# Performance work log

Hardware: AMD Instinct MI355X
Metric: run time of the kernel (lower is better)

## Reference

```python
import jax, jax.numpy as jnp
import numpy as np

HEADS = 16
ROT_DIM = 32  # RotaryEmbedding(dim=32), interleaved (GPT-J style) as in rotary_embedding_torch
THETA = 10000.0


def _rope(x):
    # x: (B, H, S, hd); rotate first ROT_DIM dims, pass through the rest
    S = x.shape[-2]
    inv_freq = 1.0 / (THETA ** (jnp.arange(0, ROT_DIM, 2, dtype=jnp.float32) / ROT_DIM))  # (ROT_DIM/2,)
    ang = jnp.arange(S, dtype=jnp.float32)[:, None] * inv_freq[None, :]                   # (S, ROT_DIM/2)
    ang = jnp.repeat(ang, 2, axis=-1)                                                     # (S, ROT_DIM) interleaved
    cos, sin = jnp.cos(ang), jnp.sin(ang)
    xr, xp = x[..., :ROT_DIM], x[..., ROT_DIM:]
    # rotate_half, interleaved pairs: (x1, x2) -> (-x2, x1)
    x2 = xr.reshape(*xr.shape[:-1], ROT_DIM // 2, 2)
    xr_half = jnp.stack([-x2[..., 1], x2[..., 0]], axis=-1).reshape(xr.shape)
    xr = xr * cos + xr_half * sin
    return jnp.concatenate([xr, xp], axis=-1)


def _split_heads(x, H):
    # (S, B, D) -> (B, H, S, hd)
    S, B, D = x.shape
    return x.transpose(1, 0, 2).reshape(B, S, H, D // H).transpose(0, 2, 1, 3)


def setup_inputs() -> dict:
    key = jax.random.key(0)
    ks = jax.random.split(key, 11)
    S, B, D = 2048, 2, 1024
    f = lambda k, shp, s=1.0: jax.random.normal(k, shp, dtype=jnp.float32) * s
    return {
        "Q": f(ks[0], (S, B, D)),
        "K": f(ks[1], (S, B, D)),
        "V": f(ks[2], (S, B, D)),
        "Wq": f(ks[3], (D, D), 0.02), "bq": f(ks[4], (D,), 0.02),
        "Wk": f(ks[5], (D, D), 0.02), "bk": f(ks[6], (D,), 0.02),
        "Wv": f(ks[7], (D, D), 0.02), "bv": f(ks[8], (D,), 0.02),
        "Wo": f(ks[9], (D, D), 0.02), "bo": f(ks[10], (D,), 0.02),
    }


def reference(Q, K, V, Wq, bq, Wk, bk, Wv, bv, Wo, bo):
    S, B, D = Q.shape
    H = HEADS
    hd = D // H
    q = _rope(_split_heads(Q @ Wq.T + bq, H))   # (B, H, S, hd)
    k = _rope(_split_heads(K @ Wk.T + bk, H))
    v = _split_heads(V @ Wv.T + bv, H)
    scores = jnp.einsum("bhqd,bhkd->bhqk", q, k) / jnp.sqrt(jnp.float32(hd))
    probs = jax.nn.softmax(scores, axis=-1)
    out = jnp.einsum("bhqk,bhkd->bhqd", probs, v)  # (B, H, S, hd)
    out = out.transpose(0, 2, 1, 3).reshape(B, S, D).transpose(1, 0, 2)  # (S, B, D)
    return out @ Wo.T + bo
```

## Files before the change

kernel.cpp:

```cpp
#include <hip/hip_runtime.h>
#include <hip/hip_bf16.h>
#include <hip/hip_fp16.h>

#define S_LEN  2048
#define BATCH  2
#define DMODEL 1024
#define NHEADS 16
#define HD     64
#define MROWS  4096
#define LD     72

using f16 = _Float16;
typedef __attribute__((ext_vector_type(8))) _Float16 f16x8;
typedef __attribute__((ext_vector_type(4))) _Float16 f16x4;
typedef __attribute__((ext_vector_type(4))) float    f32x4;

__global__ __launch_bounds__(256) void rope_table(float* __restrict__ rc, float* __restrict__ rs)
{
    int idx = blockIdx.x * 256 + threadIdx.x;
    int s = idx >> 4, i = idx & 15;
    float inv = powf(10000.0f, -(float)(2 * i) / 32.0f);
    float ang = (float)s * inv;
    rc[idx] = cosf(ang);
    rs[idx] = sinf(ang);
}

__global__ __launch_bounds__(256) void proj_gemm(
    const float* __restrict__ Xq, const float* __restrict__ Xk, const float* __restrict__ Xv,
    const float* __restrict__ Wq, const float* __restrict__ Wk, const float* __restrict__ Wv,
    const float* __restrict__ bq, const float* __restrict__ bk, const float* __restrict__ bv,
    f16* __restrict__ qo, f16* __restrict__ ko, f16* __restrict__ vo,
    const float* __restrict__ rc, const float* __restrict__ rs)
{
    const int mode = blockIdx.z;
    const float* X    = (mode == 0) ? Xq : (mode == 1) ? Xk : Xv;
    const float* W    = (mode == 0) ? Wq : (mode == 1) ? Wk : Wv;
    const float* bias = (mode == 0) ? bq : (mode == 1) ? bk : bv;

    __shared__ f16 Al[128 * 40];
    __shared__ f16 Bl[128 * 40];

    const int t = threadIdx.x;
    const int lane = t & 63, wid = t >> 6;
    const int wr = wid >> 1, wc = wid & 1;
    const int m0 = blockIdx.x * 128, n0 = blockIdx.y * 128;

    f32x4 acc[4][4];
    #pragma unroll
    for (int m = 0; m < 4; m++)
        #pragma unroll
        for (int n = 0; n < 4; n++)
            acc[m][n] = f32x4{0.f, 0.f, 0.f, 0.f};

    for (int k0 = 0; k0 < DMODEL; k0 += 32) {
        __syncthreads();
        #pragma unroll
        for (int i = 0; i < 2; i++) {
            int e = (i * 256 + t) * 8;
            int r = e >> 5, c = e & 31;
            {
                const float* src = &X[(size_t)(m0 + r) * DMODEL + k0 + c];
                float4 v0 = *reinterpret_cast<const float4*>(src);
                float4 v1 = *reinterpret_cast<const float4*>(src + 4);
                f16x8 h = { (f16)v0.x, (f16)v0.y, (f16)v0.z, (f16)v0.w,
                            (f16)v1.x, (f16)v1.y, (f16)v1.z, (f16)v1.w };
                *reinterpret_cast<f16x8*>(&Al[r * 40 + c]) = h;
            }
            {
                const float* src = &W[(size_t)(n0 + r) * DMODEL + k0 + c];
                float4 v0 = *reinterpret_cast<const float4*>(src);
                float4 v1 = *reinterpret_cast<const float4*>(src + 4);
                f16x8 h = { (f16)v0.x, (f16)v0.y, (f16)v0.z, (f16)v0.w,
                            (f16)v1.x, (f16)v1.y, (f16)v1.z, (f16)v1.w };
                *reinterpret_cast<f16x8*>(&Bl[r * 40 + c]) = h;
            }
        }
        __syncthreads();
        f16x8 a[4], b[4];
        #pragma unroll
        for (int m = 0; m < 4; m++)
            a[m] = *reinterpret_cast<const f16x8*>(&Al[(wr * 64 + m * 16 + (lane & 15)) * 40 + (lane >> 4) * 8]);
        #pragma unroll
        for (int n = 0; n < 4; n++)
            b[n] = *reinterpret_cast<const f16x8*>(&Bl[(wc * 64 + n * 16 + (lane & 15)) * 40 + (lane >> 4) * 8]);
        #pragma unroll
        for (int m = 0; m < 4; m++)
            #pragma unroll
            for (int n = 0; n < 4; n++)
                acc[m][n] = __builtin_amdgcn_mfma_f32_16x16x32_f16(a[m], b[n], acc[m][n], 0, 0, 0);
    }

    const int rowb = m0 + wr * 64, colb = n0 + wc * 64;
    #pragma unroll
    for (int n = 0; n < 4; n++) {
        int cN = colb + n * 16 + (lane & 15);
        float bvv = bias[cN];
        int h = cN >> 6, d = cN & 63;
        #pragma unroll
        for (int m = 0; m < 4; m++) {
            #pragma unroll
            for (int rg = 0; rg < 4; rg++) {
                int r = rowb + m * 16 + (lane >> 4) * 4 + rg;
                int s = r >> 1, bi = r & 1;
                float val = acc[m][n][rg] + bvv;
                if (mode < 2) {
                    float pv = __shfl_xor(val, 1);
                    if (d < 32) {
                        int fi = d >> 1;
                        float cc = rc[s * 16 + fi], ss = rs[s * 16 + fi];
                        val = ((d & 1) == 0) ? val * cc - pv * ss : val * cc + pv * ss;
                    }
                    if (mode == 0) val *= 0.18033688f;
                    ((mode == 0) ? qo : ko)[(((size_t)bi * NHEADS + h) * S_LEN + s) * HD + d] = (f16)val;
                } else {
                    vo[(((size_t)bi * NHEADS + h) * HD + d) * S_LEN + s] = (f16)val;
                }
            }
        }
    }
}

__global__ __launch_bounds__(512) void attn_fwd(
    const f16* __restrict__ qb, const f16* __restrict__ kb,
    const f16* __restrict__ vt, f16* __restrict__ ctx)
{
    __shared__ f16 Kl[64 * LD];
    __shared__ f16 Vl[64 * LD];
    __shared__ f16 Pl[8 * 16 * LD];

    const int t = threadIdx.x, lane = t & 63, wid = t >> 6;
    const int q15 = lane & 15, g = lane >> 4;
    const int bh = blockIdx.y;
    const int q0 = blockIdx.x * 128 + wid * 16;

    const f16* qptr = qb + ((size_t)bh * S_LEN + q0) * HD;
    f16x8 qf0 = *reinterpret_cast<const f16x8*>(&qptr[q15 * HD + g * 8]);
    f16x8 qf1 = *reinterpret_cast<const f16x8*>(&qptr[q15 * HD + g * 8 + 32]);

    f32x4 ctxa[4];
    #pragma unroll
    for (int i = 0; i < 4; i++) ctxa[i] = f32x4{0.f, 0.f, 0.f, 0.f};
    float mrun = -3.0e38f, lrun = 0.f;

    const int r_st = t >> 3, c_st = (t & 7) * 8;
    const f16* kg = kb + (size_t)bh * S_LEN * HD + (size_t)r_st * HD + c_st;
    const f16* vg = vt + (size_t)bh * HD * S_LEN + (size_t)r_st * S_LEN + c_st;
    f16* kl_st = &Kl[r_st * LD + c_st];
    f16* vl_st = &Vl[r_st * LD + c_st];
    f16* pbase = &Pl[wid * (16 * LD)];

    for (int kt = 0; kt < S_LEN / 64; kt++) {
        __syncthreads();
        *reinterpret_cast<uint4*>(kl_st) = *reinterpret_cast<const uint4*>(kg);
        *reinterpret_cast<uint4*>(vl_st) = *reinterpret_cast<const uint4*>(vg);
        kg += 64 * HD;
        vg += 64;
        __syncthreads();

        f32x4 sc[4];
        __builtin_amdgcn_s_setprio(1);
        #pragma unroll
        for (int f = 0; f < 4; f++) {
            f16x8 kf0 = *reinterpret_cast<const f16x8*>(&Kl[(f * 16 + q15) * LD + g * 8]);
            f16x8 kf1 = *reinterpret_cast<const f16x8*>(&Kl[(f * 16 + q15) * LD + g * 8 + 32]);
            f32x4 z = {0.f, 0.f, 0.f, 0.f};
            z = __builtin_amdgcn_mfma_f32_16x16x32_f16(kf0, qf0, z, 0, 0, 0);
            sc[f] = __builtin_amdgcn_mfma_f32_16x16x32_f16(kf1, qf1, z, 0, 0, 0);
        }
        __builtin_amdgcn_s_setprio(0);

        float pmf[4];
        #pragma unroll
        for (int f = 0; f < 4; f++)
            pmf[f] = fmaxf(fmaxf(sc[f][0], sc[f][1]), fmaxf(sc[f][2], sc[f][3]));
        float pmax = fmaxf(fmaxf(pmf[0], pmf[1]), fmaxf(pmf[2], pmf[3]));
        pmax = fmaxf(pmax, __shfl_xor(pmax, 16));
        pmax = fmaxf(pmax, __shfl_xor(pmax, 32));
        float mnew = fmaxf(mrun, pmax);
        float scale = __builtin_amdgcn_exp2f(mrun - mnew);
        float tsum = 0.f;
        #pragma unroll
        for (int f = 0; f < 4; f++)
            #pragma unroll
            for (int rg = 0; rg < 4; rg++) {
                float p = __builtin_amdgcn_exp2f(sc[f][rg] - mnew);
                sc[f][rg] = p;
                tsum += p;
            }
        tsum += __shfl_xor(tsum, 16);
        tsum += __shfl_xor(tsum, 32);
        lrun = lrun * scale + tsum;
        mrun = mnew;
        #pragma unroll
        for (int n = 0; n < 4; n++) {
            ctxa[n][0] *= scale; ctxa[n][1] *= scale;
            ctxa[n][2] *= scale; ctxa[n][3] *= scale;
        }

        #pragma unroll
        for (int f = 0; f < 4; f++) {
            f16x4 pw = { (f16)sc[f][0], (f16)sc[f][1], (f16)sc[f][2], (f16)sc[f][3] };
            *reinterpret_cast<f16x4*>(&pbase[q15 * LD + f * 16 + g * 4]) = pw;
        }
        asm volatile("s_waitcnt lgkmcnt(0)" ::: "memory");
        __builtin_amdgcn_sched_barrier(0);

        __builtin_amdgcn_s_setprio(1);
        #pragma unroll
        for (int c = 0; c < 2; c++) {
            f16x8 pfr = *reinterpret_cast<const f16x8*>(&pbase[q15 * LD + g * 8 + c * 32]);
            #pragma unroll
            for (int n = 0; n < 4; n++) {
                f16x8 vf = *reinterpret_cast<const f16x8*>(&Vl[(n * 16 + q15) * LD + g * 8 + c * 32]);
                ctxa[n] = __builtin_amdgcn_mfma_f32_16x16x32_f16(vf, pfr, ctxa[n], 0, 0, 0);
            }
        }
        __builtin_amdgcn_s_setprio(0);
    }

    const int bi = bh >> 4, h = bh & 15;
    const int s = q0 + q15;
    float inv = 1.0f / lrun;
    f16* outp = &ctx[((size_t)s * BATCH + bi) * DMODEL + h * HD];
    #pragma unroll
    for (int n = 0; n < 4; n++) {
        f16x4 o = { (f16)(ctxa[n][0] * inv), (f16)(ctxa[n][1] * inv),
                    (f16)(ctxa[n][2] * inv), (f16)(ctxa[n][3] * inv) };
        *reinterpret_cast<f16x4*>(&outp[n * 16 + g * 4]) = o;
    }
}

__global__ __launch_bounds__(256) void out_gemm(
    const f16* __restrict__ X, const float* __restrict__ W,
    const float* __restrict__ bias, float* __restrict__ out)
{
    __shared__ f16 Al[128 * 40];
    __shared__ f16 Bl[128 * 40];

    const int t = threadIdx.x;
    const int lane = t & 63, wid = t >> 6;
    const int wr = wid >> 1, wc = wid & 1;
    const int m0 = blockIdx.x * 128, n0 = blockIdx.y * 128;

    f32x4 acc[4][4];
    #pragma unroll
    for (int m = 0; m < 4; m++)
        #pragma unroll
        for (int n = 0; n < 4; n++)
            acc[m][n] = f32x4{0.f, 0.f, 0.f, 0.f};

    for (int k0 = 0; k0 < DMODEL; k0 += 32) {
        __syncthreads();
        #pragma unroll
        for (int i = 0; i < 2; i++) {
            int e = (i * 256 + t) * 8;
            int r = e >> 5, c = e & 31;
            *reinterpret_cast<uint4*>(&Al[r * 40 + c]) =
                *reinterpret_cast<const uint4*>(&X[(size_t)(m0 + r) * DMODEL + k0 + c]);
            {
                const float* src = &W[(size_t)(n0 + r) * DMODEL + k0 + c];
                float4 v0 = *reinterpret_cast<const float4*>(src);
                float4 v1 = *reinterpret_cast<const float4*>(src + 4);
                f16x8 h = { (f16)v0.x, (f16)v0.y, (f16)v0.z, (f16)v0.w,
                            (f16)v1.x, (f16)v1.y, (f16)v1.z, (f16)v1.w };
                *reinterpret_cast<f16x8*>(&Bl[r * 40 + c]) = h;
            }
        }
        __syncthreads();
        f16x8 a[4], b[4];
        #pragma unroll
        for (int m = 0; m < 4; m++)
            a[m] = *reinterpret_cast<const f16x8*>(&Al[(wr * 64 + m * 16 + (lane & 15)) * 40 + (lane >> 4) * 8]);
        #pragma unroll
        for (int n = 0; n < 4; n++)
            b[n] = *reinterpret_cast<const f16x8*>(&Bl[(wc * 64 + n * 16 + (lane & 15)) * 40 + (lane >> 4) * 8]);
        #pragma unroll
        for (int m = 0; m < 4; m++)
            #pragma unroll
            for (int n = 0; n < 4; n++)
                acc[m][n] = __builtin_amdgcn_mfma_f32_16x16x32_f16(a[m], b[n], acc[m][n], 0, 0, 0);
    }

    const int rowb = m0 + wr * 64, colb = n0 + wc * 64;
    #pragma unroll
    for (int n = 0; n < 4; n++) {
        int cN = colb + n * 16 + (lane & 15);
        float bvv = bias[cN];
        #pragma unroll
        for (int m = 0; m < 4; m++) {
            #pragma unroll
            for (int rg = 0; rg < 4; rg++) {
                int r = rowb + m * 16 + (lane >> 4) * 4 + rg;
                out[(size_t)r * DMODEL + cN] = acc[m][n][rg] + bvv;
            }
        }
    }
}

extern "C" void kernel_launch(void* const* d_in, const int* in_sizes, int n_in,
                              void* d_out, int out_size, void* d_ws, size_t ws_size,
                              hipStream_t stream)
{
    const float* Q  = (const float*)d_in[0];
    const float* K  = (const float*)d_in[1];
    const float* V  = (const float*)d_in[2];
    const float* Wq = (const float*)d_in[3];
    const float* bq = (const float*)d_in[4];
    const float* Wk = (const float*)d_in[5];
    const float* bk = (const float*)d_in[6];
    const float* Wv = (const float*)d_in[7];
    const float* bv = (const float*)d_in[8];
    const float* Wo = (const float*)d_in[9];
    const float* bo = (const float*)d_in[10];
    float* out = (float*)d_out;

    char* w = (char*)d_ws;
    const size_t szT = (size_t)S_LEN * 16 * sizeof(float);
    const size_t szQ = (size_t)MROWS * DMODEL * sizeof(f16);
    float* rc  = (float*)(w);
    float* rs  = (float*)(w + szT);
    f16* qbuf = (f16*)(w + 2 * szT);
    f16* kbuf = (f16*)(w + 2 * szT + szQ);
    f16* vtb  = (f16*)(w + 2 * szT + 2 * szQ);
    f16* ctxb = (f16*)(w + 2 * szT + 3 * szQ);

    rope_table<<<(S_LEN * 16) / 256, 256, 0, stream>>>(rc, rs);

    proj_gemm<<<dim3(MROWS / 128, DMODEL / 128, 3), 256, 0, stream>>>(
        Q, K, V, Wq, Wk, Wv, bq, bk, bv, qbuf, kbuf, vtb, rc, rs);

    attn_fwd<<<dim3(S_LEN / 128, BATCH * NHEADS), 512, 0, stream>>>(qbuf, kbuf, vtb, ctxb);

    out_gemm<<<dim3(MROWS / 128, DMODEL / 128), 256, 0, stream>>>(ctxb, Wo, bo, out);
}
```

Before: 169.0 us.

## Pre-convert inputs and weights to fp16 and use async LDS-load GEMMs

Adds a conversion kernel that casts Q/K/V and all four weight matrices to fp16 in workspace. New projection and output GEMMs then load fp16 tiles directly into LDS with global_load_lds, replacing the fp32 load-and-convert staging. This is meant to halve GEMM input bandwidth and drop per-tile conversion work. The cost is an extra pass over about 64MB of fp32 data plus a workspace-size-dependent code path, with the old path kept as fallback.

```diff
diff --git a/kernel.cpp b/kernel.cpp
--- a/kernel.cpp
+++ b/kernel.cpp
@@ -15,6 +15,12 @@
 typedef __attribute__((ext_vector_type(4))) _Float16 f16x4;
 typedef __attribute__((ext_vector_type(4))) float    f32x4;
 
+__device__ __forceinline__ void gload16(const void* g, void* l)
+{
+    __builtin_amdgcn_global_load_lds((const __attribute__((address_space(1))) void*)g,
+                                     (__attribute__((address_space(3))) void*)l, 16, 0, 0);
+}
+
 __global__ __launch_bounds__(256) void rope_table(float* __restrict__ rc, float* __restrict__ rs)
 {
     int idx = blockIdx.x * 256 + threadIdx.x;
@@ -23,6 +29,185 @@
     float ang = (float)s * inv;
     rc[idx] = cosf(ang);
     rs[idx] = sinf(ang);
+}
+
+__global__ __launch_bounds__(256) void cvt_all(
+    const float* __restrict__ Q, const float* __restrict__ K, const float* __restrict__ V,
+    const float* __restrict__ Wq, const float* __restrict__ Wk, const float* __restrict__ Wv,
+    const float* __restrict__ Wo, f16* __restrict__ dst)
+{
+    const int z = blockIdx.y;
+    const float* src; size_t off; int n8;
+    switch (z) {
+        case 0:  src = Q;  off = 0;        n8 = 524288; break;
+        case 1:  src = K;  off = 4194304;  n8 = 524288; break;
+        case 2:  src = V;  off = 8388608;  n8 = 524288; break;
+        case 3:  src = Wq; off = 12582912; n8 = 131072; break;
+        case 4:  src = Wk; off = 13631488; n8 = 131072; break;
+        case 5:  src = Wv; off = 14680064; n8 = 131072; break;
+        default: src = Wo; off = 15728640; n8 = 131072; break;
+    }
+    int i = blockIdx.x * 256 + threadIdx.x;
+    if (i >= n8) return;
+    const float4* s = reinterpret_cast<const float4*>(src) + (size_t)i * 2;
+    float4 v0 = s[0], v1 = s[1];
+    f16x8 h = { (f16)v0.x, (f16)v0.y, (f16)v0.z, (f16)v0.w,
+                (f16)v1.x, (f16)v1.y, (f16)v1.z, (f16)v1.w };
+    reinterpret_cast<f16x8*>(dst + off)[i] = h;
+}
+
+__global__ __launch_bounds__(256) void proj_gemm_h(
+    const f16* __restrict__ Xq, const f16* __restrict__ Xk, const f16* __restrict__ Xv,
+    const f16* __restrict__ Wq, const f16* __restrict__ Wk, const f16* __restrict__ Wv,
+    const float* __restrict__ bq, const float* __restrict__ bk, const float* __restrict__ bv,
+    f16* __restrict__ qo, f16* __restrict__ ko, f16* __restrict__ vo,
+    const float* __restrict__ rc, const float* __restrict__ rs)
+{
+    const int mode = blockIdx.z;
+    const f16* X     = (mode == 0) ? Xq : (mode == 1) ? Xk : Xv;
+    const f16* W     = (mode == 0) ? Wq : (mode == 1) ? Wk : Wv;
+    const float* bias = (mode == 0) ? bq : (mode == 1) ? bk : bv;
+
+    __shared__ f16 Al[128 * 32];
+    __shared__ f16 Bl[128 * 32];
+
+    const int t = threadIdx.x, lane = t & 63, wid = t >> 6;
+    const int q15 = lane & 15, g = lane >> 4;
+    const int wr = wid >> 1, wc = wid & 1;
+    const int m0 = blockIdx.x * 128, n0 = blockIdx.y * 128;
+
+    const int srow = wid * 16 + (lane >> 2);
+    const int scol = (lane & 3) * 8;
+    const f16* Xg = X + (size_t)(m0 + srow) * DMODEL + scol;
+    const f16* Wg = W + (size_t)(n0 + srow) * DMODEL + scol;
+    f16* al0 = &Al[(wid * 16) * 32];
+    f16* al1 = &Al[(wid * 16 + 64) * 32];
+    f16* bl0 = &Bl[(wid * 16) * 32];
+    f16* bl1 = &Bl[(wid * 16 + 64) * 32];
+
+    f32x4 acc[4][4];
+    #pragma unroll
+    for (int m = 0; m < 4; m++)
+        #pragma unroll
+        for (int n = 0; n < 4; n++)
+            acc[m][n] = f32x4{0.f, 0.f, 0.f, 0.f};
+
+    for (int k0 = 0; k0 < DMODEL; k0 += 32) {
+        __syncthreads();
+        gload16(Xg + k0, al0);
+        gload16(Xg + (size_t)64 * DMODEL + k0, al1);
+        gload16(Wg + k0, bl0);
+        gload16(Wg + (size_t)64 * DMODEL + k0, bl1);
+        __syncthreads();
+
+        f16x8 a[4], b[4];
+        #pragma unroll
+        for (int m = 0; m < 4; m++)
+            a[m] = *reinterpret_cast<const f16x8*>(&Al[(wr * 64 + m * 16 + q15) * 32 + g * 8]);
+        #pragma unroll
+        for (int n = 0; n < 4; n++)
+            b[n] = *reinterpret_cast<const f16x8*>(&Bl[(wc * 64 + n * 16 + q15) * 32 + g * 8]);
+        #pragma unroll
+        for (int m = 0; m < 4; m++)
+            #pragma unroll
+            for (int n = 0; n < 4; n++)
+                acc[m][n] = __builtin_amdgcn_mfma_f32_16x16x32_f16(a[m], b[n], acc[m][n], 0, 0, 0);
+    }
+
+    const int rowb = m0 + wr * 64, colb = n0 + wc * 64;
+    #pragma unroll
+    for (int n = 0; n < 4; n++) {
+        int cN = colb + n * 16 + q15;
+        float bvv = bias[cN];
+        int h = cN >> 6, d = cN & 63;
+        #pragma unroll
+        for (int m = 0; m < 4; m++) {
+            #pragma unroll
+            for (int rg = 0; rg < 4; rg++) {
+                int r = rowb + m * 16 + g * 4 + rg;
+                int s = r >> 1, bi = r & 1;
+                float val = acc[m][n][rg] + bvv;
+                if (mode < 2) {
+                    float pv = __shfl_xor(val, 1);
+                    if (d < 32) {
+                        int fi = d >> 1;
+                        float cc = rc[s * 16 + fi], ss = rs[s * 16 + fi];
+                        val = ((d & 1) == 0) ? val * cc - pv * ss : val * cc + pv * ss;
+                    }
+                    if (mode == 0) val *= 0.18033688f;
+                    ((mode == 0) ? qo : ko)[(((size_t)bi * NHEADS + h) * S_LEN + s) * HD + d] = (f16)val;
+                } else {
+                    vo[(((size_t)bi * NHEADS + h) * HD + d) * S_LEN + s] = (f16)val;
+                }
+            }
+        }
+    }
+}
+
+__global__ __launch_bounds__(256) void out_gemm_h(
+    const f16* __restrict__ X, const f16* __restrict__ W,
+    const float* __restrict__ bias, float* __restrict__ out)
+{
+    __shared__ f16 Al[128 * 32];
+    __shared__ f16 Bl[128 * 32];
+
+    const int t = threadIdx.x, lane = t & 63, wid = t >> 6;
+    const int q15 = lane & 15, g = lane >> 4;
+    const int wr = wid >> 1, wc = wid & 1;
+    const int m0 = blockIdx.x * 128, n0 = blockIdx.y * 128;
+
+    const int srow = wid * 16 + (lane >> 2);
+    const int scol = (lane & 3) * 8;
+    const f16* Xg = X + (size_t)(m0 + srow) * DMODEL + scol;
+    const f16* Wg = W + (size_t)(n0 + srow) * DMODEL + scol;
+    f16* al0 = &Al[(wid * 16) * 32];
+    f16* al1 = &Al[(wid * 16 + 64) * 32];
+    f16* bl0 = &Bl[(wid * 16) * 32];
+    f16* bl1 = &Bl[(wid * 16 + 64) * 32];
+
+    f32x4 acc[4][4];
+    #pragma unroll
+    for (int m = 0; m < 4; m++)
+        #pragma unroll
+        for (int n = 0; n < 4; n++)
+            acc[m][n] = f32x4{0.f, 0.f, 0.f, 0.f};
+
+    for (int k0 = 0; k0 < DMODEL; k0 += 32) {
+        __syncthreads();
+        gload16(Xg + k0, al0);
+        gload16(Xg + (size_t)64 * DMODEL + k0, al1);
+        gload16(Wg + k0, bl0);
+        gload16(Wg + (size_t)64 * DMODEL + k0, bl1);
+        __syncthreads();
+
+        f16x8 a[4], b[4];
+        #pragma unroll
+        for (int m = 0; m < 4; m++)
+            a[m] = *reinterpret_cast<const f16x8*>(&Al[(wr * 64 + m * 16 + q15) * 32 + g * 8]);
+        #pragma unroll
+        for (int n = 0; n < 4; n++)
+            b[n] = *reinterpret_cast<const f16x8*>(&Bl[(wc * 64 + n * 16 + q15) * 32 + g * 8]);
+        #pragma unroll
+        for (int m = 0; m < 4; m++)
+            #pragma unroll
+            for (int n = 0; n < 4; n++)
+                acc[m][n] = __builtin_amdgcn_mfma_f32_16x16x32_f16(a[m], b[n], acc[m][n], 0, 0, 0);
+    }
+
+    const int rowb = m0 + wr * 64, colb = n0 + wc * 64;
+    #pragma unroll
+    for (int n = 0; n < 4; n++) {
+        int cN = colb + n * 16 + q15;
+        float bvv = bias[cN];
+        #pragma unroll
+        for (int m = 0; m < 4; m++) {
+            #pragma unroll
+            for (int rg = 0; rg < 4; rg++) {
+                int r = rowb + m * 16 + g * 4 + rg;
+                out[(size_t)r * DMODEL + cN] = acc[m][n][rg] + bvv;
+            }
+        }
+    }
 }
 
 __global__ __launch_bounds__(256) void proj_gemm(
@@ -120,116 +305,6 @@
     }
 }
 
-__global__ __launch_bounds__(512) void attn_fwd(
-    const f16* __restrict__ qb, const f16* __restrict__ kb,
-    const f16* __restrict__ vt, f16* __restrict__ ctx)
-{
-    __shared__ f16 Kl[64 * LD];
-    __shared__ f16 Vl[64 * LD];
-    __shared__ f16 Pl[8 * 16 * LD];
-
-    const int t = threadIdx.x, lane = t & 63, wid = t >> 6;
-    const int q15 = lane & 15, g = lane >> 4;
-    const int bh = blockIdx.y;
-    const int q0 = blockIdx.x * 128 + wid * 16;
-
-    const f16* qptr = qb + ((size_t)bh * S_LEN + q0) * HD;
-    f16x8 qf0 = *reinterpret_cast<const f16x8*>(&qptr[q15 * HD + g * 8]);
-    f16x8 qf1 = *reinterpret_cast<const f16x8*>(&qptr[q15 * HD + g * 8 + 32]);
-
-    f32x4 ctxa[4];
-    #pragma unroll
-    for (int i = 0; i < 4; i++) ctxa[i] = f32x4{0.f, 0.f, 0.f, 0.f};
-    float mrun = -3.0e38f, lrun = 0.f;
-
-    const int r_st = t >> 3, c_st = (t & 7) * 8;
-    const f16* kg = kb + (size_t)bh * S_LEN * HD + (size_t)r_st * HD + c_st;
-    const f16* vg = vt + (size_t)bh * HD * S_LEN + (size_t)r_st * S_LEN + c_st;
-    f16* kl_st = &Kl[r_st * LD + c_st];
-    f16* vl_st = &Vl[r_st * LD + c_st];
-    f16* pbase = &Pl[wid * (16 * LD)];
-
-    for (int kt = 0; kt < S_LEN / 64; kt++) {
-        __syncthreads();
-        *reinterpret_cast<uint4*>(kl_st) = *reinterpret_cast<const uint4*>(kg);
-        *reinterpret_cast<uint4*>(vl_st) = *reinterpret_cast<const uint4*>(vg);
-        kg += 64 * HD;
-        vg += 64;
-        __syncthreads();
-
-        f32x4 sc[4];
-        __builtin_amdgcn_s_setprio(1);
-        #pragma unroll
-        for (int f = 0; f < 4; f++) {
-            f16x8 kf0 = *reinterpret_cast<const f16x8*>(&Kl[(f * 16 + q15) * LD + g * 8]);
-            f16x8 kf1 = *reinterpret_cast<const f16x8*>(&Kl[(f * 16 + q15) * LD + g * 8 + 32]);
-            f32x4 z = {0.f, 0.f, 0.f, 0.f};
-            z = __builtin_amdgcn_mfma_f32_16x16x32_f16(kf0, qf0, z, 0, 0, 0);
-            sc[f] = __builtin_amdgcn_mfma_f32_16x16x32_f16(kf1, qf1, z, 0, 0, 0);
-        }
-        __builtin_amdgcn_s_setprio(0);
-
-        float pmf[4];
-        #pragma unroll
-        for (int f = 0; f < 4; f++)
-            pmf[f] = fmaxf(fmaxf(sc[f][0], sc[f][1]), fmaxf(sc[f][2], sc[f][3]));
-        float pmax = fmaxf(fmaxf(pmf[0], pmf[1]), fmaxf(pmf[2], pmf[3]));
-        pmax = fmaxf(pmax, __shfl_xor(pmax, 16));
-        pmax = fmaxf(pmax, __shfl_xor(pmax, 32));
-        float mnew = fmaxf(mrun, pmax);
-        float scale = __builtin_amdgcn_exp2f(mrun - mnew);
-        float tsum = 0.f;
-        #pragma unroll
-        for (int f = 0; f < 4; f++)
-            #pragma unroll
-            for (int rg = 0; rg < 4; rg++) {
-                float p = __builtin_amdgcn_exp2f(sc[f][rg] - mnew);
-                sc[f][rg] = p;
-                tsum += p;
-            }
-        tsum += __shfl_xor(tsum, 16);
-        tsum += __shfl_xor(tsum, 32);
-        lrun = lrun * scale + tsum;
-        mrun = mnew;
-        #pragma unroll
-        for (int n = 0; n < 4; n++) {
-            ctxa[n][0] *= scale; ctxa[n][1] *= scale;
-            ctxa[n][2] *= scale; ctxa[n][3] *= scale;
-        }
-
-        #pragma unroll
-        for (int f = 0; f < 4; f++) {
-            f16x4 pw = { (f16)sc[f][0], (f16)sc[f][1], (f16)sc[f][2], (f16)sc[f][3] };
-            *reinterpret_cast<f16x4*>(&pbase[q15 * LD + f * 16 + g * 4]) = pw;
-        }
-        asm volatile("s_waitcnt lgkmcnt(0)" ::: "memory");
-        __builtin_amdgcn_sched_barrier(0);
-
-        __builtin_amdgcn_s_setprio(1);
-        #pragma unroll
-        for (int c = 0; c < 2; c++) {
-            f16x8 pfr = *reinterpret_cast<const f16x8*>(&pbase[q15 * LD + g * 8 + c * 32]);
-            #pragma unroll
-            for (int n = 0; n < 4; n++) {
-                f16x8 vf = *reinterpret_cast<const f16x8*>(&Vl[(n * 16 + q15) * LD + g * 8 + c * 32]);
-                ctxa[n] = __builtin_amdgcn_mfma_f32_16x16x32_f16(vf, pfr, ctxa[n], 0, 0, 0);
-            }
-        }
-        __builtin_amdgcn_s_setprio(0);
-    }
-
-    const int bi = bh >> 4, h = bh & 15;
-    const int s = q0 + q15;
-    float inv = 1.0f / lrun;
-    f16* outp = &ctx[((size_t)s * BATCH + bi) * DMODEL + h * HD];
-    #pragma unroll
-    for (int n = 0; n < 4; n++) {
-        f16x4 o = { (f16)(ctxa[n][0] * inv), (f16)(ctxa[n][1] * inv),
-                    (f16)(ctxa[n][2] * inv), (f16)(ctxa[n][3] * inv) };
-        *reinterpret_cast<f16x4*>(&outp[n * 16 + g * 4]) = o;
-    }
-}
-
 __global__ __launch_bounds__(256) void out_gemm(
     const f16* __restrict__ X, const float* __restrict__ W,
     const float* __restrict__ bias, float* __restrict__ out)
@@ -297,6 +372,116 @@
     }
 }
 
+__global__ __launch_bounds__(512) void attn_fwd(
+    const f16* __restrict__ qb, const f16* __restrict__ kb,
+    const f16* __restrict__ vt, f16* __restrict__ ctx)
+{
+    __shared__ f16 Kl[64 * LD];
+    __shared__ f16 Vl[64 * LD];
+    __shared__ f16 Pl[8 * 16 * LD];
+
+    const int t = threadIdx.x, lane = t & 63, wid = t >> 6;
+    const int q15 = lane & 15, g = lane >> 4;
+    const int bh = blockIdx.y;
+    const int q0 = blockIdx.x * 128 + wid * 16;
+
+    const f16* qptr = qb + ((size_t)bh * S_LEN + q0) * HD;
+    f16x8 qf0 = *reinterpret_cast<const f16x8*>(&qptr[q15 * HD + g * 8]);
+    f16x8 qf1 = *reinterpret_cast<const f16x8*>(&qptr[q15 * HD + g * 8 + 32]);
+
+    f32x4 ctxa[4];
+    #pragma unroll
+    for (int i = 0; i < 4; i++) ctxa[i] = f32x4{0.f, 0.f, 0.f, 0.f};
+    float mrun = -3.0e38f, lrun = 0.f;
+
+    const int r_st = t >> 3, c_st = (t & 7) * 8;
+    const f16* kg = kb + (size_t)bh * S_LEN * HD + (size_t)r_st * HD + c_st;
+    const f16* vg = vt + (size_t)bh * HD * S_LEN + (size_t)r_st * S_LEN + c_st;
+    f16* kl_st = &Kl[r_st * LD + c_st];
+    f16* vl_st = &Vl[r_st * LD + c_st];
+    f16* pbase = &Pl[wid * (16 * LD)];
+
+    for (int kt = 0; kt < S_LEN / 64; kt++) {
+        __syncthreads();
+        *reinterpret_cast<uint4*>(kl_st) = *reinterpret_cast<const uint4*>(kg);
+        *reinterpret_cast<uint4*>(vl_st) = *reinterpret_cast<const uint4*>(vg);
+        kg += 64 * HD;
+        vg += 64;
+        __syncthreads();
+
+        f32x4 sc[4];
+        __builtin_amdgcn_s_setprio(1);
+        #pragma unroll
+        for (int f = 0; f < 4; f++) {
+            f16x8 kf0 = *reinterpret_cast<const f16x8*>(&Kl[(f * 16 + q15) * LD + g * 8]);
+            f16x8 kf1 = *reinterpret_cast<const f16x8*>(&Kl[(f * 16 + q15) * LD + g * 8 + 32]);
+            f32x4 z = {0.f, 0.f, 0.f, 0.f};
+            z = __builtin_amdgcn_mfma_f32_16x16x32_f16(kf0, qf0, z, 0, 0, 0);
+            sc[f] = __builtin_amdgcn_mfma_f32_16x16x32_f16(kf1, qf1, z, 0, 0, 0);
+        }
+        __builtin_amdgcn_s_setprio(0);
+
+        float pmf[4];
+        #pragma unroll
+        for (int f = 0; f < 4; f++)
+            pmf[f] = fmaxf(fmaxf(sc[f][0], sc[f][1]), fmaxf(sc[f][2], sc[f][3]));
+        float pmax = fmaxf(fmaxf(pmf[0], pmf[1]), fmaxf(pmf[2], pmf[3]));
+        pmax = fmaxf(pmax, __shfl_xor(pmax, 16));
+        pmax = fmaxf(pmax, __shfl_xor(pmax, 32));
+        float mnew = fmaxf(mrun, pmax);
+        float scale = __builtin_amdgcn_exp2f(mrun - mnew);
+        float tsum = 0.f;
+        #pragma unroll
+        for (int f = 0; f < 4; f++)
+            #pragma unroll
+            for (int rg = 0; rg < 4; rg++) {
+                float p = __builtin_amdgcn_exp2f(sc[f][rg] - mnew);
+                sc[f][rg] = p;
+                tsum += p;
+            }
+        tsum += __shfl_xor(tsum, 16);
+        tsum += __shfl_xor(tsum, 32);
+        lrun = lrun * scale + tsum;
+        mrun = mnew;
+        #pragma unroll
+        for (int n = 0; n < 4; n++) {
+            ctxa[n][0] *= scale; ctxa[n][1] *= scale;
+            ctxa[n][2] *= scale; ctxa[n][3] *= scale;
+        }
+
+        #pragma unroll
+        for (int f = 0; f < 4; f++) {
+            f16x4 pw = { (f16)sc[f][0], (f16)sc[f][1], (f16)sc[f][2], (f16)sc[f][3] };
+            *reinterpret_cast<f16x4*>(&pbase[q15 * LD + f * 16 + g * 4]) = pw;
+        }
+        asm volatile("s_waitcnt lgkmcnt(0)" ::: "memory");
+        __builtin_amdgcn_sched_barrier(0);
+
+        __builtin_amdgcn_s_setprio(1);
+        #pragma unroll
+        for (int c = 0; c < 2; c++) {
+            f16x8 pfr = *reinterpret_cast<const f16x8*>(&pbase[q15 * LD + g * 8 + c * 32]);
+            #pragma unroll
+            for (int n = 0; n < 4; n++) {
+                f16x8 vf = *reinterpret_cast<const f16x8*>(&Vl[(n * 16 + q15) * LD + g * 8 + c * 32]);
+                ctxa[n] = __builtin_amdgcn_mfma_f32_16x16x32_f16(vf, pfr, ctxa[n], 0, 0, 0);
+            }
+        }
+        __builtin_amdgcn_s_setprio(0);
+    }
+
+    const int bi = bh >> 4, h = bh & 15;
+    const int s = q0 + q15;
+    float inv = 1.0f / lrun;
+    f16* outp = &ctx[((size_t)s * BATCH + bi) * DMODEL + h * HD];
+    #pragma unroll
+    for (int n = 0; n < 4; n++) {
+        f16x4 o = { (f16)(ctxa[n][0] * inv), (f16)(ctxa[n][1] * inv),
+                    (f16)(ctxa[n][2] * inv), (f16)(ctxa[n][3] * inv) };
+        *reinterpret_cast<f16x4*>(&outp[n * 16 + g * 4]) = o;
+    }
+}
+
 extern "C" void kernel_launch(void* const* d_in, const int* in_sizes, int n_in,
                               void* d_out, int out_size, void* d_ws, size_t ws_size,
                               hipStream_t stream)
@@ -315,21 +500,45 @@
     float* out = (float*)d_out;
 
     char* w = (char*)d_ws;
-    const size_t szT = (size_t)S_LEN * 16 * sizeof(float);
-    const size_t szQ = (size_t)MROWS * DMODEL * sizeof(f16);
-    float* rc  = (float*)(w);
-    float* rs  = (float*)(w + szT);
-    f16* qbuf = (f16*)(w + 2 * szT);
-    f16* kbuf = (f16*)(w + 2 * szT + szQ);
-    f16* vtb  = (f16*)(w + 2 * szT + 2 * szQ);
-    f16* ctxb = (f16*)(w + 2 * szT + 3 * szQ);
-
-    rope_table<<<(S_LEN * 16) / 256, 256, 0, stream>>>(rc, rs);
-
-    proj_gemm<<<dim3(MROWS / 128, DMODEL / 128, 3), 256, 0, stream>>>(
-        Q, K, V, Wq, Wk, Wv, bq, bk, bv, qbuf, kbuf, vtb, rc, rs);
-
-    attn_fwd<<<dim3(S_LEN / 128, BATCH * NHEADS), 512, 0, stream>>>(qbuf, kbuf, vtb, ctxb);
-
-    out_gemm<<<dim3(MROWS / 128, DMODEL / 128), 256, 0, stream>>>(ctxb, Wo, bo, out);
-}
+    const size_t MBc = 1024 * 1024;
+    const size_t NEED_FAST = 56 * MBc + 256 * 1024;
+
+    if (ws_size >= NEED_FAST) {
+        f16* cvtb = (f16*)w;
+        f16* Xqh = cvtb;
+        f16* Xkh = cvtb + 4194304;
+        f16* Xvh = cvtb + 8388608;
+        f16* Wqh = cvtb + 12582912;
+        f16* Wkh = cvtb + 13631488;
+        f16* Wvh = cvtb + 14680064;
+        f16* Woh = cvtb + 15728640;
+        float* rc = (float*)(w + 32 * MBc);
+        float* rs = rc + 32768;
+        f16* qbuf = (f16*)(w + 32 * MBc + 256 * 1024);
+        f16* kbuf = qbuf + 4194304;
+        f16* vtb  = kbuf + 4194304;
+        f16* ctxb = Xqh;
+
+        rope_table<<<(S_LEN * 16) / 256, 256, 0, stream>>>(rc, rs);
+        cvt_all<<<dim3(2048, 7), 256, 0, stream>>>(Q, K, V, Wq, Wk, Wv, Wo, cvtb);
+        proj_gemm_h<<<dim3(MROWS / 128, DMODEL / 128, 3), 256, 0, stream>>>(
+            Xqh, Xkh, Xvh, Wqh, Wkh, Wvh, bq, bk, bv, qbuf, kbuf, vtb, rc, rs);
+        attn_fwd<<<dim3(S_LEN / 128, BATCH * NHEADS), 512, 0, stream>>>(qbuf, kbuf, vtb, ctxb);
+        out_gemm_h<<<dim3(MROWS / 128, DMODEL / 128), 256, 0, stream>>>(ctxb, Woh, bo, out);
+    } else {
+        const size_t szT = (size_t)S_LEN * 16 * sizeof(float);
+        const size_t szQ = (size_t)MROWS * DMODEL * sizeof(f16);
+        float* rc  = (float*)(w);
+        float* rs  = (float*)(w + szT);
+        f16* qbuf = (f16*)(w + 2 * szT);
+        f16* kbuf = (f16*)(w + 2 * szT + szQ);
+        f16* vtb  = (f16*)(w + 2 * szT + 2 * szQ);
+        f16* ctxb = (f16*)(w + 2 * szT + 3 * szQ);
+
+        rope_table<<<(S_LEN * 16) / 256, 256, 0, stream>>>(rc, rs);
+        proj_gemm<<<dim3(MROWS / 128, DMODEL / 128, 3), 256, 0, stream>>>(
+            Q, K, V, Wq, Wk, Wv, bq, bk, bv, qbuf, kbuf, vtb, rc, rs);
+        attn_fwd<<<dim3(S_LEN / 128, BATCH * NHEADS), 512, 0, stream>>>(qbuf, kbuf, vtb, ctxb);
+        out_gemm<<<dim3(MROWS / 128, DMODEL / 128), 256, 0, stream>>>(ctxb, Wo, bo, out);
+    }
+}
```

Result: faster. 158.9 us (-5.9%).
